# Kernel tuning notes

Measured on AMD Instinct MI355X. Metric: run time of the kernel, lower is better.

Reference implementation:

```python
import jax, jax.numpy as jnp
import numpy as np
from jax import lax

B, SEQ, PRED, CIN = 32, 336, 336, 7
ALL = SEQ + PRED
DM, DFF, NFFT, WIN, HOP = 64, 64, 64, 64, 8
NF = ALL // HOP + 1  # 85 STFT frames (center=True)
EL, CL, MARK = 2, 3, 4


def _conv2d(x, w, b, dil, pad):
    y = lax.conv_general_dilated(x, w, (1, 1), [(pad, pad), (pad, pad)],
                                 rhs_dilation=(dil, dil),
                                 dimension_numbers=('NCHW', 'OIHW', 'NCHW'))
    return y + b[None, :, None, None]


def _cconv(xr, xi, wr, wi, br, bi, dil, pad):
    # complex conv: (conv_r + i*conv_i)(xr + i*xi)
    rr = _conv2d(xr, wr, br, dil, pad)
    ii = _conv2d(xi, wi, bi, dil, pad)
    ri = _conv2d(xi, wr, br, dil, pad)
    ir = _conv2d(xr, wi, bi, dil, pad)
    return rr - ii, ri + ir


def _block(x, p):
    # x: [B, ALL, DM]; STFT per channel series (vectorized over B*DM, no python batch loop)
    xp = jnp.pad(x.transpose(0, 2, 1), ((0, 0), (0, 0), (NFFT // 2, NFFT // 2)), mode='reflect')
    idx = jnp.arange(NF)[:, None] * HOP + jnp.arange(NFFT)[None, :]
    win = 0.5 - 0.5 * jnp.cos(2.0 * jnp.pi * jnp.arange(WIN, dtype=jnp.float32) / WIN)  # periodic hann
    frames = xp[:, :, idx] * win  # [B, DM, NF, NFFT]
    S = jnp.fft.fft(frames, axis=-1) / jnp.sqrt(jnp.float32(NFFT))  # normalized=True (ortho)
    Sr = S.real.transpose(0, 1, 3, 2).astype(jnp.float32)  # [B, DM, NFFT, NF]
    Si = S.imag.transpose(0, 1, 3, 2).astype(jnp.float32)
    # complex 'qk' attention: compl_mul1d('ijxk,ijyk->ijxy', S, S)
    qk_r = jnp.einsum('bnxk,bnyk->bnxy', Sr, Sr) - jnp.einsum('bnxk,bnyk->bnxy', Si, Si)
    qk_i = jnp.einsum('bnxk,bnyk->bnxy', Sr, Si) + jnp.einsum('bnxk,bnyk->bnxy', Si, Sr)
    g_r = jax.nn.sigmoid(qk_r)
    g_i = jax.nn.sigmoid(qk_i)
    ar = jnp.einsum('bnxy,bnyz->bnxz', g_r, Sr) - jnp.einsum('bnxy,bnyz->bnxz', g_i, Si)
    ai = jnp.einsum('bnxy,bnyz->bnxz', g_r, Si) + jnp.einsum('bnxy,bnyz->bnxz', g_i, Sr)
    outs_r, outs_i = [], []
    yr, yi = _cconv(ar, ai, p['c0_wr'], p['c0_wi'], p['c0_br'], p['c0_bi'], 1, 0)
    outs_r.append(jax.nn.relu(yr)); outs_i.append(jax.nn.relu(yi))
    for k in range(1, CL):
        hr, hi = _cconv(ar, ai, p['cA_wr'][k - 1], p['cA_wi'][k - 1], p['cA_br'][k - 1], p['cA_bi'][k - 1], k, k)
        yr, yi = _cconv(hr, hi, p['cB_wr'][k - 1], p['cB_wi'][k - 1], p['cB_br'][k - 1], p['cB_bi'][k - 1], k, k)
        outs_r.append(jax.nn.relu(yr)); outs_i.append(jax.nn.relu(yi))
    mr = jnp.mean(jnp.stack(outs_r, -1), -1)
    mi = jnp.mean(jnp.stack(outs_i, -1), -1)
    y = mr * p['l0_w'][0, 0] + mi * p['l0_w'][0, 1] + p['l0_b'][0]  # Linear(2 -> 1) over (real, imag)
    y = y.mean(axis=2)  # mean over freq axis -> [B, DM, NF]
    y = jnp.einsum('bnf,af->bna', y, p['l2_w']) + p['l2_b']  # l2: NF -> ALL
    return y.transpose(0, 2, 1)  # [B, ALL, DM]


def _ln(x, g, b):
    m = x.mean(-1, keepdims=True)
    v = ((x - m) ** 2).mean(-1, keepdims=True)
    return (x - m) / jnp.sqrt(v + 1e-5) * g + b


def _forward(x_enc, x_mark_enc, tok_w, temp_w, pl_w, pl_b, ln_g, ln_b,
             c0_wr, c0_wi, c0_br, c0_bi, cA_wr, cA_wi, cA_br, cA_bi,
             cB_wr, cB_wi, cB_br, cB_bi, l0_w, l0_b, l2_w, l2_b,
             cv_w, cv_b, l1_w, l1_b, proj_w, proj_b):
    means = x_enc.mean(1, keepdims=True)
    xe = x_enc - means
    stdev = jnp.sqrt(xe.var(axis=1, keepdims=True) + 1e-5)
    xe = xe / stdev
    # DataEmbedding: circular token conv + sinusoidal PE + timeF linear (dropout=0)
    xv = jnp.pad(xe.transpose(0, 2, 1), ((0, 0), (0, 0), (1, 1)), mode='wrap')
    val = lax.conv_general_dilated(xv, tok_w, (1,), [(0, 0)],
                                   dimension_numbers=('NCH', 'OIH', 'NCH')).transpose(0, 2, 1)
    pos = jnp.arange(SEQ, dtype=jnp.float32)[:, None]
    div = jnp.exp(jnp.arange(0, DM, 2, dtype=jnp.float32) * (-np.log(10000.0) / DM))
    pe = jnp.zeros((SEQ, DM), jnp.float32).at[:, 0::2].set(jnp.sin(pos * div)).at[:, 1::2].set(jnp.cos(pos * div))
    enc = val + x_mark_enc @ temp_w.T + pe
    enc = jnp.einsum('btd,at->bad', enc, pl_w) + pl_b[None, :, None]  # predict_linear over time axis
    for l in range(EL):
        p = dict(c0_wr=c0_wr[l], c0_wi=c0_wi[l], c0_br=c0_br[l], c0_bi=c0_bi[l],
                 cA_wr=cA_wr[l], cA_wi=cA_wi[l], cA_br=cA_br[l], cA_bi=cA_bi[l],
                 cB_wr=cB_wr[l], cB_wi=cB_wi[l], cB_br=cB_br[l], cB_bi=cB_bi[l],
                 l0_w=l0_w[l], l0_b=l0_b[l], l2_w=l2_w[l], l2_b=l2_b[l])
        enc = _ln(_block(enc, p), ln_g, ln_b)
    # conv1d(in=ALL channels, kernel 3, stride 2, pad 1) over the d_model axis, then l1
    h = lax.conv_general_dilated(enc, cv_w, (2,), [(1, 1)],
                                 dimension_numbers=('NCH', 'OIH', 'NCH')) + cv_b[None, :, None]
    seq_series = (h @ l1_w.T)[..., 0] + l1_b[0]  # [B, ALL]
    dec = enc @ proj_w.T + proj_b
    dec = dec * stdev + means
    return dec[:, -PRED:, :], seq_series


def setup_inputs():
    key = jax.random.key(0)
    ks = jax.random.split(key, 24)
    def r(i, shape, s=0.02):
        return jax.random.normal(ks[i], shape, dtype=jnp.float32) * s
    return {
        'x_enc': jax.random.normal(ks[0], (B, SEQ, CIN), dtype=jnp.float32),
        'x_mark_enc': jax.random.normal(ks[1], (B, SEQ, MARK), dtype=jnp.float32),
        'x_dec': jax.random.normal(ks[2], (B, 48 + PRED, CIN), dtype=jnp.float32),
        'x_mark_dec': jax.random.normal(ks[3], (B, 48 + PRED, MARK), dtype=jnp.float32),
        'tok_w': r(4, (DM, CIN, 3), 0.1),
        'temp_w': r(5, (DM, MARK), 0.1),
        'pl_w': r(6, (ALL, SEQ), 0.05),
        'pl_b': jnp.zeros((ALL,), jnp.float32),
        'ln_g': jnp.ones((DM,), jnp.float32),
        'ln_b': jnp.zeros((DM,), jnp.float32),
        'c0_wr': r(7, (EL, DM, DM, 1, 1), 0.05),
        'c0_wi': r(8, (EL, DM, DM, 1, 1), 0.05),
        'c0_br': jnp.zeros((EL, DM), jnp.float32),
        'c0_bi': jnp.zeros((EL, DM), jnp.float32),
        'cA_wr': r(9, (EL, CL - 1, DFF, DM, 3, 3), 0.02),
        'cA_wi': r(10, (EL, CL - 1, DFF, DM, 3, 3), 0.02),
        'cA_br': jnp.zeros((EL, CL - 1, DFF), jnp.float32),
        'cA_bi': jnp.zeros((EL, CL - 1, DFF), jnp.float32),
        'cB_wr': r(11, (EL, CL - 1, DM, DFF, 3, 3), 0.02),
        'cB_wi': r(12, (EL, CL - 1, DM, DFF, 3, 3), 0.02),
        'cB_br': jnp.zeros((EL, CL - 1, DM), jnp.float32),
        'cB_bi': jnp.zeros((EL, CL - 1, DM), jnp.float32),
        'l0_w': r(13, (EL, 1, 2), 0.5),
        'l0_b': jnp.zeros((EL, 1), jnp.float32),
        'l2_w': r(14, (EL, ALL, NF), 0.05),
        'l2_b': jnp.zeros((EL, ALL), jnp.float32),
        'cv_w': r(15, (ALL, ALL, 3), 0.02),
        'cv_b': jnp.zeros((ALL,), jnp.float32),
        'l1_w': r(16, (1, DM // 2), 0.1),
        'l1_b': jnp.zeros((1,), jnp.float32),
        'proj_w': r(17, (CIN, DM), 0.1),
        'proj_b': jnp.zeros((CIN,), jnp.float32),
    }


def reference(x_enc, x_mark_enc, x_dec, x_mark_dec, tok_w, temp_w, pl_w, pl_b, ln_g, ln_b,
              c0_wr, c0_wi, c0_br, c0_bi, cA_wr, cA_wi, cA_br, cA_bi,
              cB_wr, cB_wi, cB_br, cB_bi, l0_w, l0_b, l2_w, l2_b,
              cv_w, cv_b, l1_w, l1_b, proj_w, proj_b):
    del x_dec, x_mark_dec  # unused in the forecast path
    return _forward(x_enc, x_mark_enc, tok_w, temp_w, pl_w, pl_b, ln_g, ln_b,
                    c0_wr, c0_wi, c0_br, c0_bi, cA_wr, cA_wi, cA_br, cA_bi,
                    cB_wr, cB_wi, cB_br, cB_bi, l0_w, l0_b, l2_w, l2_b,
                    cv_w, cv_b, l1_w, l1_b, proj_w, proj_b)
```

## Files before the change

### kernel.cpp

```cpp
#include <hip/hip_runtime.h>

typedef __attribute__((ext_vector_type(8))) short short8v;
typedef __attribute__((ext_vector_type(4))) float f32x4;
typedef __attribute__((ext_vector_type(16))) float f32x16;

static constexpr int Bt = 32;
static constexpr int SEQ = 336, PRED = 336, CIN = 7, ALLT = 672;
static constexpr int DM = 64, NFFT = 64, HOP = 8, NF = 85;
static constexpr int FPAD = 100;
static constexpr int MARK = 4;
static constexpr float INV3 = 1.0f / 3.0f;

__device__ inline short f2bf(float v) {
    unsigned u = __float_as_uint(v);
    u += 0x7fffu + ((u >> 16) & 1u);
    return (short)(u >> 16);
}
__device__ inline float bf2f(short h) {
    return __uint_as_float(((unsigned)(unsigned short)h) << 16);
}
__device__ inline int pack2(float r, float i) {
    return ((int)(unsigned short)f2bf(r)) | (((int)(unsigned short)f2bf(i)) << 16);
}
__device__ inline void async16(const int* g, short* l) {
    __builtin_amdgcn_global_load_lds(
        (const __attribute__((address_space(1))) unsigned int*)g,
        (__attribute__((address_space(3))) unsigned int*)l, 16, 0, 0);
}

__global__ __launch_bounds__(64) void k_stats(const float* __restrict__ x,
                                              float* __restrict__ mean,
                                              float* __restrict__ stdv) {
    int bc = blockIdx.x;
    int b = bc / CIN, c = bc % CIN;
    int lane = threadIdx.x;
    float s = 0.f, s2 = 0.f;
    for (int t = lane; t < SEQ; t += 64) {
        float v = x[(b * SEQ + t) * CIN + c];
        s += v; s2 += v * v;
    }
    for (int m = 32; m >= 1; m >>= 1) { s += __shfl_xor(s, m); s2 += __shfl_xor(s2, m); }
    if (lane == 0) {
        float mu = s / SEQ;
        float var = s2 / SEQ - mu * mu;
        mean[bc] = mu;
        stdv[bc] = sqrtf(var + 1e-5f);
    }
}

__global__ __launch_bounds__(256) void k_embed(const float* __restrict__ x,
                                               const float* __restrict__ mark,
                                               const float* __restrict__ tok_w,
                                               const float* __restrict__ temp_w,
                                               const float* __restrict__ mean,
                                               const float* __restrict__ stdv,
                                               float* __restrict__ enc0) {
    int i = blockIdx.x * 256 + threadIdx.x;
    if (i >= Bt * SEQ * DM) return;
    int d = i & 63;
    int t = (i >> 6) % SEQ;
    int b = i / (SEQ * DM);
    float val = 0.f;
    for (int c = 0; c < CIN; ++c) {
        float mu = mean[b * CIN + c];
        float is = 1.f / stdv[b * CIN + c];
        for (int j = 0; j < 3; ++j) {
            int tt = t + j - 1;
            if (tt < 0) tt += SEQ;
            if (tt >= SEQ) tt -= SEQ;
            float xv = (x[(b * SEQ + tt) * CIN + c] - mu) * is;
            val += xv * tok_w[(d * CIN + c) * 3 + j];
        }
    }
    float mk = 0.f;
    for (int m = 0; m < MARK; ++m) mk += mark[(b * SEQ + t) * MARK + m] * temp_w[d * MARK + m];
    float div = expf(-(float)(d & ~1) * (9.210340371976184f / (float)DM));
    float arg = (float)t * div;
    float pe = (d & 1) ? cosf(arg) : sinf(arg);
    enc0[i] = val + mk + pe;
}

__global__ __launch_bounds__(256) void k_plin2(const float* __restrict__ enc0,
                                               const float* __restrict__ pl_w,
                                               const float* __restrict__ pl_b,
                                               float* __restrict__ enc) {
    __shared__ float Et[56 * 64];
    __shared__ float Wt[56 * 49];
    int blk = blockIdx.x;
    int b = blk / 14, at = blk % 14;
    int abase = at * 48;
    int tid = threadIdx.x;
    int a0 = (tid & 15) * 3;
    int d0 = (tid >> 4) * 4;
    float acc[3][4];
#pragma unroll
    for (int q = 0; q < 3; ++q)
#pragma unroll
        for (int r = 0; r < 4; ++r) acc[q][r] = 0.f;
    for (int tc = 0; tc < 6; ++tc) {
        if (tc) __syncthreads();
        for (int i = tid; i < 56 * 64; i += 256)
            Et[i] = enc0[((size_t)b * SEQ + tc * 56) * DM + i];
        for (int i = tid; i < 48 * 56; i += 256) {
            int r = i / 56, c = i - r * 56;
            Wt[c * 49 + r] = pl_w[(size_t)(abase + r) * SEQ + tc * 56 + c];
        }
        __syncthreads();
#pragma unroll 4
        for (int t = 0; t < 56; ++t) {
            float4 e = *(const float4*)&Et[t * 64 + d0];
            float w0 = Wt[t * 49 + a0];
            float w1 = Wt[t * 49 + a0 + 1];
            float w2 = Wt[t * 49 + a0 + 2];
            acc[0][0] += w0 * e.x; acc[0][1] += w0 * e.y;
            acc[0][2] += w0 * e.z; acc[0][3] += w0 * e.w;
            acc[1][0] += w1 * e.x; acc[1][1] += w1 * e.y;
            acc[1][2] += w1 * e.z; acc[1][3] += w1 * e.w;
            acc[2][0] += w2 * e.x; acc[2][1] += w2 * e.y;
            acc[2][2] += w2 * e.z; acc[2][3] += w2 * e.w;
        }
    }
#pragma unroll
    for (int q = 0; q < 3; ++q) {
        int a = abase + a0 + q;
        float bias = pl_b[a];
        float4 o = {acc[q][0] + bias, acc[q][1] + bias, acc[q][2] + bias, acc[q][3] + bias};
        *(float4*)&enc[((size_t)b * ALLT + a) * DM + d0] = o;
    }
}

__global__ __launch_bounds__(256) void k_twprep(short* __restrict__ twg) {
    int idx = blockIdx.x * 256 + threadIdx.x;
    if (idx < 18432) {
        int arr = idx / 4608;
        int rem = idx - arr * 4608;
        int k = rem / 72, tt = rem - k * 72;
        float v = 0.f;
        if (tt < 64) {
            int m = (k * tt) & 63;
            float ang = (6.283185307179586f / 64.f) * (float)m;
            float c = (arr < 2) ? cosf(ang) : sinf(ang);
            v = (arr & 1) ? (c - bf2f(f2bf(c))) : c;
        }
        twg[idx] = f2bf(v);
    } else if (idx < 18432 + 64) {
        int tt = idx - 18432;
        float ang = (6.283185307179586f / 64.f) * (float)tt;
        ((float*)(twg + 18432))[tt] = (0.5f - 0.5f * cosf(ang)) * 0.125f;
    }
}

__global__ __launch_bounds__(256) void k_encT(const float* __restrict__ enc,
                                              float* __restrict__ encT) {
    __shared__ float tile[64][65];
    int b = blockIdx.x / 11, tt0 = (blockIdx.x % 11) * 64;
    int tid = threadIdx.x;
    int tx = tid & 63, ty = tid >> 6;
    for (int r = ty; r < 64; r += 4) {
        int t = tt0 + r;
        if (t < ALLT) tile[r][tx] = enc[((size_t)b * ALLT + t) * DM + tx];
    }
    __syncthreads();
    for (int r = ty; r < 64; r += 4) {
        int t = tt0 + tx;
        if (t < ALLT) encT[((size_t)b * DM + r) * ALLT + t] = tile[tx][r];
    }
}

__global__ __launch_bounds__(256) void k_padzero(int4* __restrict__ base, int nrows) {
    int idx = blockIdx.x * 256 + threadIdx.x;
    if (idx >= nrows * 15) return;
    int r = idx / 15, p = idx - r * 15;
    int f = (p < 2) ? p : (85 + p);
    base[(size_t)r * FPAD + f] = int4{0, 0, 0, 0};
}

__global__ __launch_bounds__(512) void k_stqka(const float* __restrict__ encT, int b0,
                                               int* __restrict__ Apk,
                                               const short* __restrict__ twg) {
    __shared__ __align__(16) short L[54272];
    constexpr int TCH = 0, TCL = 4608, TSH = 9216, TSL = 13824;
    constexpr int XWH = 18432, XWL = 25344;
    float* xp  = (float*)&L[32256];
    float* win = (float*)&L[33728];
    constexpr int SRH = 0, SIH = 6656, SRL = 13312, SIL = 19968;
    constexpr int STRH = 26624, STRL = 33536, STIH = 40448, STIL = 47360;
    constexpr int GRH = 0, GRL = 4608, GIH = 9216, GIL = 13824;

    int blk = blockIdx.x;
    int bn = (blk & 7) * (gridDim.x >> 3) + (blk >> 3);
    int bl = bn >> 6, n = bn & 63;
    int bg = b0 + bl;
    int tid = threadIdx.x;
    int lane = tid & 63, w = tid >> 6;
    int l31 = lane & 31, kg = lane >> 5;

    for (int i = tid; i < ALLT + NFFT; i += 512) {
        int j = i - 32;
        if (j < 0) j = -j;
        if (j > ALLT - 1) j = 2 * (ALLT - 1) - j;
        xp[i] = encT[(size_t)(bg * 64 + n) * ALLT + j];
    }
    for (int i = tid; i < 2304; i += 512)
        *(int4*)&L[i * 8] = ((const int4*)twg)[i];
    if (tid < 64) win[tid] = ((const float*)(twg + 18432))[tid];
    __syncthreads();
    for (int i = tid; i < 96 * 64; i += 512) {
        int f = i >> 6, tt = i & 63;
        float v = 0.f;
        if (f < 85) v = xp[f * HOP + tt] * win[tt];
        short vh = f2bf(v); short vl = f2bf(v - bf2f(vh));
        int o = f * 72 + tt;
        L[XWH + o] = vh; L[XWL + o] = vl;
    }
    __syncthreads();

    int kt = w & 1, ft = w >> 1;
    f32x16 sr, si;
#pragma unroll
    for (int r = 0; r < 16; ++r) { sr[r] = 0.f; si[r] = 0.f; }
    if (w < 6) {
#pragma unroll
        for (int tts = 0; tts < 4; ++tts) {
            int ko = (kt * 32 + l31) * 72 + tts * 16 + kg * 8;
            short8v ach = *(const short8v*)&L[TCH + ko];
            short8v acl = *(const short8v*)&L[TCL + ko];
            short8v ash = *(const short8v*)&L[TSH + ko];
            short8v asl = *(const short8v*)&L[TSL + ko];
            int bo = (ft * 32 + l31) * 72 + tts * 16 + kg * 8;
            short8v bh = *(const short8v*)&L[XWH + bo];
            short8v bl_ = *(const short8v*)&L[XWL + bo];
            sr = __builtin_amdgcn_mfma_f32_32x32x16_bf16(ach, bh, sr, 0, 0, 0);
            sr = __builtin_amdgcn_mfma_f32_32x32x16_bf16(acl, bh, sr, 0, 0, 0);
            sr = __builtin_amdgcn_mfma_f32_32x32x16_bf16(ach, bl_, sr, 0, 0, 0);
            si = __builtin_amdgcn_mfma_f32_32x32x16_bf16(ash, bh, si, 0, 0, 0);
            si = __builtin_amdgcn_mfma_f32_32x32x16_bf16(asl, bh, si, 0, 0, 0);
            si = __builtin_amdgcn_mfma_f32_32x32x16_bf16(ash, bl_, si, 0, 0, 0);
        }
    }
    __syncthreads();

    if (w < 6) {
        int fA = ft * 32 + l31;
#pragma unroll
        for (int rg = 0; rg < 4; ++rg) {
            int k0 = kt * 32 + 8 * rg + 4 * kg;
            short prh[4], prl[4], pih[4], pil[4];
#pragma unroll
            for (int q = 0; q < 4; ++q) {
                int r = rg * 4 + q;
                float sv = sr[r], iv = -si[r];
                short rh = f2bf(sv); short rl = f2bf(sv - bf2f(rh));
                short ih = f2bf(iv); short il = f2bf(iv - bf2f(ih));
                prh[q] = rh; prl[q] = rl; pih[q] = ih; pil[q] = il;
                L[SRH + (k0 + q) * 104 + fA] = rh; L[SRL + (k0 + q) * 104 + fA] = rl;
                L[SIH + (k0 + q) * 104 + fA] = ih; L[SIL + (k0 + q) * 104 + fA] = il;
            }
            *(long long*)&L[STRH + fA * 72 + k0] = *(long long*)prh;
            *(long long*)&L[STRL + fA * 72 + k0] = *(long long*)prl;
            *(long long*)&L[STIH + fA * 72 + k0] = *(long long*)pih;
            *(long long*)&L[STIL + fA * 72 + k0] = *(long long*)pil;
        }
    }
    __syncthreads();

    int mh = w >> 1, nh = w & 1;
    f32x16 P, Q, R;
#pragma unroll
    for (int r = 0; r < 16; ++r) { P[r] = 0.f; Q[r] = 0.f; R[r] = 0.f; }
    if (w < 4) {
#pragma unroll
        for (int f0 = 0; f0 < 96; f0 += 16) {
            int ka = f0 + kg * 8;
            int ra = (mh * 32 + l31) * 104 + ka;
            int rb = (nh * 32 + l31) * 104 + ka;
            short8v a_rh = *(const short8v*)&L[SRH + ra];
            short8v a_rl = *(const short8v*)&L[SRL + ra];
            short8v a_ih = *(const short8v*)&L[SIH + ra];
            short8v a_il = *(const short8v*)&L[SIL + ra];
            short8v b_rh = *(const short8v*)&L[SRH + rb];
            short8v b_rl = *(const short8v*)&L[SRL + rb];
            short8v b_ih = *(const short8v*)&L[SIH + rb];
            short8v b_il = *(const short8v*)&L[SIL + rb];
            P = __builtin_amdgcn_mfma_f32_32x32x16_bf16(a_rh, b_rh, P, 0, 0, 0);
            P = __builtin_amdgcn_mfma_f32_32x32x16_bf16(a_rl, b_rh, P, 0, 0, 0);
            P = __builtin_amdgcn_mfma_f32_32x32x16_bf16(a_rh, b_rl, P, 0, 0, 0);
            Q = __builtin_amdgcn_mfma_f32_32x32x16_bf16(a_ih, b_ih, Q, 0, 0, 0);
            Q = __builtin_amdgcn_mfma_f32_32x32x16_bf16(a_il, b_ih, Q, 0, 0, 0);
            Q = __builtin_amdgcn_mfma_f32_32x32x16_bf16(a_ih, b_il, Q, 0, 0, 0);
            R = __builtin_amdgcn_mfma_f32_32x32x16_bf16(a_rh, b_ih, R, 0, 0, 0);
            R = __builtin_amdgcn_mfma_f32_32x32x16_bf16(a_rl, b_ih, R, 0, 0, 0);
            R = __builtin_amdgcn_mfma_f32_32x32x16_bf16(a_rh, b_il, R, 0, 0, 0);
            R = __builtin_amdgcn_mfma_f32_32x32x16_bf16(a_ih, b_rh, R, 0, 0, 0);
            R = __builtin_amdgcn_mfma_f32_32x32x16_bf16(a_il, b_rh, R, 0, 0, 0);
            R = __builtin_amdgcn_mfma_f32_32x32x16_bf16(a_ih, b_rl, R, 0, 0, 0);
        }
    }
    __syncthreads();

    if (w < 4) {
        int y = nh * 32 + l31;
#pragma unroll
        for (int r = 0; r < 16; ++r) {
            int x = mh * 32 + (r & 3) + 8 * (r >> 2) + 4 * kg;
            float gr = 1.f / (1.f + __expf(-(P[r] - Q[r])));
            float gi = 1.f / (1.f + __expf(-R[r]));
            short gh = f2bf(gr); short gl = f2bf(gr - bf2f(gh));
            short jh = f2bf(gi); short jl = f2bf(gi - bf2f(jh));
            L[GRH + x * 72 + y] = gh; L[GRL + x * 72 + y] = gl;
            L[GIH + x * 72 + y] = jh; L[GIL + x * 72 + y] = jl;
        }
    }
    __syncthreads();

    int mt = w >> 1, nx = w & 1;
    f32x16 u1, u2, u3;
#pragma unroll
    for (int r = 0; r < 16; ++r) { u1[r] = 0.f; u2[r] = 0.f; u3[r] = 0.f; }
    if (w < 6) {
#pragma unroll
        for (int y0 = 0; y0 < 64; y0 += 16) {
            int kb = y0 + kg * 8;
            int gb = (nx * 32 + l31) * 72 + kb;
            short8v bgrh = *(const short8v*)&L[GRH + gb];
            short8v bgrl = *(const short8v*)&L[GRL + gb];
            short8v bgih = *(const short8v*)&L[GIH + gb];
            short8v bgil = *(const short8v*)&L[GIL + gb];
            int sa = (mt * 32 + l31) * 72 + kb;
            short8v arh = *(const short8v*)&L[STRH + sa];
            short8v arl = *(const short8v*)&L[STRL + sa];
            short8v aih = *(const short8v*)&L[STIH + sa];
            short8v ail = *(const short8v*)&L[STIL + sa];
            u1 = __builtin_amdgcn_mfma_f32_32x32x16_bf16(arh, bgrh, u1, 0, 0, 0);
            u1 = __builtin_amdgcn_mfma_f32_32x32x16_bf16(arl, bgrh, u1, 0, 0, 0);
            u1 = __builtin_amdgcn_mfma_f32_32x32x16_bf16(arh, bgrl, u1, 0, 0, 0);
            u2 = __builtin_amdgcn_mfma_f32_32x32x16_bf16(aih, bgih, u2, 0, 0, 0);
            u2 = __builtin_amdgcn_mfma_f32_32x32x16_bf16(ail, bgih, u2, 0, 0, 0);
            u2 = __builtin_amdgcn_mfma_f32_32x32x16_bf16(aih, bgil, u2, 0, 0, 0);
            u3 = __builtin_amdgcn_mfma_f32_32x32x16_bf16(aih, bgrh, u3, 0, 0, 0);
            u3 = __builtin_amdgcn_mfma_f32_32x32x16_bf16(ail, bgrh, u3, 0, 0, 0);
            u3 = __builtin_amdgcn_mfma_f32_32x32x16_bf16(aih, bgrl, u3, 0, 0, 0);
            u3 = __builtin_amdgcn_mfma_f32_32x32x16_bf16(arh, bgih, u3, 0, 0, 0);
            u3 = __builtin_amdgcn_mfma_f32_32x32x16_bf16(arl, bgih, u3, 0, 0, 0);
            u3 = __builtin_amdgcn_mfma_f32_32x32x16_bf16(arh, bgil, u3, 0, 0, 0);
        }
    }
    if (w < 6) {
        size_t pkbase = ((size_t)(bl * 16 + (n >> 2)) * 64) * FPAD * 4 + (n & 3);
        int x2 = nx * 32 + l31;
#pragma unroll
        for (int r = 0; r < 16; ++r) {
            int z = mt * 32 + (r & 3) + 8 * (r >> 2) + 4 * kg;
            if (z < 85)
                Apk[pkbase + ((size_t)x2 * FPAD + z + 2) * 4] = pack2(u1[r] - u2[r], u3[r]);
        }
    }
}

__global__ __launch_bounds__(256) void k_wprep(const float* __restrict__ cA_wr,
                                               const float* __restrict__ cA_wi,
                                               const float* __restrict__ cB_wr,
                                               const float* __restrict__ cB_wi,
                                               const float* __restrict__ c0_wr,
                                               const float* __restrict__ c0_wi,
                                               short* __restrict__ wt) {
    int idx = blockIdx.x * 256 + threadIdx.x;
    if (idx >= 1245184) return;
    int c32 = idx & 31;
    int m = (idx >> 5) & 127;
    int ci_l = c32 >> 1;
    int part = c32 & 1;
    int co = m & 63;
    const float *wr, *wi;
    size_t woff;
    bool lo = false;
    int chunk;
    if (idx < 1179648) {
        chunk = (idx >> 12) & 3;
        int tap = (idx >> 14) % 9;
        int conv = idx / 147456;
        int l = conv >> 2, k1 = (conv >> 1) & 1, ab = conv & 1;
        int ci = chunk * 16 + ci_l;
        woff = (((size_t)(l * 2 + k1) * 64 + co) * 64 + ci) * 9 + tap;
        wr = ab ? cB_wr : cA_wr;
        wi = ab ? cB_wi : cA_wi;
    } else {
        int i2 = idx - 1179648;
        chunk = (i2 >> 12) & 3;
        lo = (i2 >> 14) & 1;
        int l = i2 >> 15;
        int ci = chunk * 16 + ci_l;
        woff = ((size_t)(l * 64 + co)) * 64 + ci;
        wr = c0_wr; wi = c0_wi;
    }
    float a = wr[woff], bb = wi[woff];
    float v = (m < 64) ? (part ? -bb : a) : (part ? a : bb);
    if (lo) v = v - bf2f(f2bf(v));
    wt[idx] = f2bf(v);
}

__global__ __launch_bounds__(256, 4) void k_conv3p(const int* __restrict__ in_pk,
                                                   const short* __restrict__ wt,
                                                   const float* __restrict__ b_r,
                                                   const float* __restrict__ b_i,
                                                   int K, int mode,
                                                   const float* __restrict__ l0w,
                                                   int* __restrict__ out_pk,
                                                   float* __restrict__ yfull) {
    __shared__ __align__(16) short inT[2][1200 * 8];
    int blk = blockIdx.x;
    int swz = (blk & 7) * (gridDim.x >> 3) + (blk >> 3);
    int b = swz >> 6, x0 = swz & 63;
    int tid = threadIdx.x;
    int lane = tid & 63, wid = tid >> 6;
    int wrow = wid & 1, wcol = wid >> 1;
    int l15 = lane & 15, g = lane >> 4;

#define STAGE(CC, BUFI)                                                       \
    do {                                                                      \
        _Pragma("unroll")                                                     \
        for (int it = 0; it < 5; ++it) {                                      \
            int idx = tid + it * 256;                                         \
            if (idx < 1200) {                                                 \
                int f = idx % FPAD;                                           \
                int rc = idx / FPAD;                                          \
                int xr = rc >> 2, cg = rc & 3;                                \
                int xg = x0 + (xr - 1) * K;                                   \
                if ((unsigned)xg < 64u) {                                     \
                    const int* src = in_pk +                                  \
                        (((size_t)((b * 16 + (CC) * 4 + cg) * 64 + xg)) * FPAD + f) * 4; \
                    async16(src, &inT[BUFI][(wid * 64 + it * 256) * 8]);      \
                }                                                             \
            }                                                                 \
        }                                                                     \
    } while (0)

    { int* p = (int*)&inT[0][0];
      for (int i = tid; i < 2 * 1200 * 4; i += 256) p[i] = 0; }
    __syncthreads();

    f32x4 acc[4][3];
#pragma unroll
    for (int a = 0; a < 4; ++a)
#pragma unroll
        for (int j = 0; j < 3; ++j) acc[a][j] = f32x4{0.f, 0.f, 0.f, 0.f};

    STAGE(0, 0);
    __syncthreads();

    int cur = 0;
    for (int chunk = 0; chunk < 4; ++chunk) {
        if (chunk == 0) STAGE(1, 1);
        else if (chunk == 1) STAGE(2, 0);
        else if (chunk == 2) STAGE(3, 1);
        const short* bb = &inT[cur][0];
#pragma unroll
        for (int u = 0; u < 3; ++u) {
#pragma unroll
            for (int v = 0; v < 3; ++v) {
                int tap = u * 3 + v;
                short8v afr[4];
#pragma unroll
                for (int a = 0; a < 4; ++a) {
                    int tile = (a < 2) ? (wrow * 2 + a) : (wrow * 2 + a + 2);
                    const short* ap = wt + ((((size_t)tap * 4 + chunk) * 8 + tile) * 16 + l15) * 32 + g * 8;
                    afr[a] = *(const short8v*)ap;
                }
                short8v bfr[3];
#pragma unroll
                for (int j = 0; j < 3; ++j) {
                    int fs2 = (wcol * 3 + j) * 16 + l15 + (v - 1) * K + 2;
                    bfr[j] = *(const short8v*)&bb[((u * 4 + g) * FPAD + fs2) * 8];
                }
#pragma unroll
                for (int a = 0; a < 4; ++a)
#pragma unroll
                    for (int j = 0; j < 3; ++j)
                        acc[a][j] = __builtin_amdgcn_mfma_f32_16x16x32_bf16(afr[a], bfr[j],
                                                                            acc[a][j], 0, 0, 0);
            }
        }
        __syncthreads();
        cur ^= 1;
    }
#undef STAGE

    float w0 = 0.f, w1 = 0.f;
    if (mode == 1) { w0 = l0w[0]; w1 = l0w[1]; }
#pragma unroll
    for (int a = 0; a < 2; ++a) {
#pragma unroll
        for (int j = 0; j < 3; ++j) {
            int f = (wcol * 3 + j) * 16 + l15;
            if (f < NF) {
                if (mode == 0) {
                    int4 o;
#pragma unroll
                    for (int reg = 0; reg < 4; ++reg) {
                        int co = (wrow * 2 + a) * 16 + g * 4 + reg;
                        float vrq = acc[a][j][reg]     + b_r[co] - b_i[co];
                        float viq = acc[a + 2][j][reg] + b_r[co] + b_i[co];
                        ((int*)&o)[reg] = pack2(vrq, viq);
                    }
                    int co4 = (wrow * 2 + a) * 4 + g;
                    ((int4*)out_pk)[((size_t)((b * 16 + co4) * 64 + x0)) * FPAD + f + 2] = o;
                } else {
#pragma unroll
                    for (int reg = 0; reg < 4; ++reg) {
                        int co = (wrow * 2 + a) * 16 + g * 4 + reg;
                        float vrq = acc[a][j][reg]     + b_r[co] - b_i[co];
                        float viq = acc[a + 2][j][reg] + b_r[co] + b_i[co];
                        size_t o = ((size_t)(b * 64 + co) * 64 + x0) * NF + f;
                        yfull[o] += (fmaxf(vrq, 0.f) * w0 + fmaxf(viq, 0.f) * w1) * INV3;
                    }
                }
            }
        }
    }
}

__global__ __launch_bounds__(256, 4) void k_c0m(const int* __restrict__ Apk,
                                                const short* __restrict__ wt,
                                                const float* __restrict__ b_r,
                                                const float* __restrict__ b_i,
                                                const float* __restrict__ l0w,
                                                float* __restrict__ yfull) {
    __shared__ __align__(16) short inT[100 * 40];
    int blk = blockIdx.x;
    int swz = (blk & 7) * (gridDim.x >> 3) + (blk >> 3);
    int b = swz >> 6, x0 = swz & 63;
    int tid = threadIdx.x;
    int lane = tid & 63, wid = tid >> 6;
    int wrow = wid & 1, wcol = wid >> 1;
    int l15 = lane & 15, g = lane >> 4;

    f32x4 acc[4][3];
#pragma unroll
    for (int a = 0; a < 4; ++a)
#pragma unroll
        for (int j = 0; j < 3; ++j) acc[a][j] = f32x4{0.f, 0.f, 0.f, 0.f};

    for (int chunk = 0; chunk < 4; ++chunk) {
        if (chunk > 0) __syncthreads();
        for (int idx = tid; idx < 400; idx += 256) {
            int f = idx % FPAD;
            int cg = idx / FPAD;
            size_t s4 = ((size_t)((b * 16 + chunk * 4 + cg) * 64 + x0)) * FPAD + f;
            int4 dh = ((const int4*)Apk)[s4];
            *(int4*)&inT[f * 40 + cg * 8] = dh;
        }
        __syncthreads();
#pragma unroll
        for (int wtap = 0; wtap < 2; ++wtap) {
            short8v afr[4];
#pragma unroll
            for (int a = 0; a < 4; ++a) {
                int tile = (a < 2) ? (wrow * 2 + a) : (wrow * 2 + a + 2);
                const short* ap = wt + ((((size_t)wtap * 4 + chunk) * 8 + tile) * 16 + l15) * 32 + g * 8;
                afr[a] = *(const short8v*)ap;
            }
            short8v bfr[3];
#pragma unroll
            for (int j = 0; j < 3; ++j) {
                int fs = (wcol * 3 + j) * 16 + l15 + 2;
                bfr[j] = *(const short8v*)&inT[fs * 40 + g * 8];
            }
#pragma unroll
            for (int a = 0; a < 4; ++a)
#pragma unroll
                for (int j = 0; j < 3; ++j)
                    acc[a][j] = __builtin_amdgcn_mfma_f32_16x16x32_bf16(afr[a], bfr[j],
                                                                        acc[a][j], 0, 0, 0);
        }
    }

    float w0 = l0w[0], w1 = l0w[1];
#pragma unroll
    for (int a = 0; a < 2; ++a) {
#pragma unroll
        for (int j = 0; j < 3; ++j) {
            int f = (wcol * 3 + j) * 16 + l15;
            if (f < NF) {
#pragma unroll
                for (int reg = 0; reg < 4; ++reg) {
                    int co = (wrow * 2 + a) * 16 + g * 4 + reg;
                    float vrq = acc[a][j][reg]     + b_r[co] - b_i[co];
                    float viq = acc[a + 2][j][reg] + b_r[co] + b_i[co];
                    size_t o = ((size_t)(b * 64 + co) * 64 + x0) * NF + f;
                    yfull[o] = (fmaxf(vrq, 0.f) * w0 + fmaxf(viq, 0.f) * w1) * INV3;
                }
            }
        }
    }
}

__global__ __launch_bounds__(256) void k_reduce2(const float* __restrict__ yfull,
                                                 const float* __restrict__ l0b,
                                                 float* __restrict__ y2) {
    __shared__ float fs[3][85];
    int bn = blockIdx.x;
    int tid = threadIdx.x;
    const float* p = yfull + (size_t)bn * 64 * 85;
    if (tid < 255) {
        int f = tid % 85, g = tid / 85;
        float s = 0.f;
        for (int x = g; x < 64; x += 3) s += p[x * 85 + f];
        fs[g][f] = s;
    }
    __syncthreads();
    if (tid < 85)
        y2[(size_t)bn * 85 + tid] = (fs[0][tid] + fs[1][tid] + fs[2][tid]) * (1.f / 64.f) + l0b[0];
}

__global__ __launch_bounds__(64) void k_l2ln(const float* __restrict__ y2,
                                             const float* __restrict__ l2w,
                                             const float* __restrict__ l2b,
                                             const float* __restrict__ g,
                                             const float* __restrict__ be,
                                             float* __restrict__ enc, int b0) {
    int bl = blockIdx.x / ALLT;
    int a = blockIdx.x % ALLT;
    int d = threadIdx.x;
    const float* wp = l2w + (size_t)a * NF;
    const float* yp = y2 + (size_t)(bl * 64 + d) * NF;
    float acc = l2b[a];
    for (int f = 0; f < NF; ++f) acc += yp[f] * wp[f];
    float s = acc, s2 = acc * acc;
    for (int m = 32; m >= 1; m >>= 1) { s += __shfl_xor(s, m); s2 += __shfl_xor(s2, m); }
    float mu = s * (1.f / 64.f);
    float var = s2 * (1.f / 64.f) - mu * mu;
    float rs = rsqrtf(var + 1e-5f);
    enc[((size_t)(b0 + bl) * ALLT + a) * DM + d] = (acc - mu) * rs * g[d] + be[d];
}

__global__ __launch_bounds__(256) void k_T(const float* __restrict__ enc,
                                           const float* __restrict__ l1w,
                                           float* __restrict__ T) {
    int i = blockIdx.x * 256 + threadIdx.x;
    if (i >= Bt * ALLT * 3) return;
    int j = i % 3;
    int rest = i / 3;
    int ci = rest % ALLT;
    int b = rest / ALLT;
    const float* e = enc + ((size_t)b * ALLT + ci) * DM;
    float s = 0.f;
    for (int hx = 0; hx < 32; ++hx) {
        int p = 2 * hx + j - 1;
        if (p >= 0 && p < DM) s += e[p] * l1w[hx];
    }
    T[i] = s;
}

__global__ __launch_bounds__(256) void k_seq(const float* __restrict__ T,
                                             const float* __restrict__ cvw,
                                             const float* __restrict__ cvb,
                                             const float* __restrict__ l1w,
                                             const float* __restrict__ l1b,
                                             float* __restrict__ out) {
    int i = blockIdx.x * 256 + threadIdx.x;
    if (i >= Bt * ALLT) return;
    int co = i % ALLT;
    int b = i / ALLT;
    float sl1 = 0.f;
    for (int hx = 0; hx < 32; ++hx) sl1 += l1w[hx];
    const float* tp = T + (size_t)b * ALLT * 3;
    const float* wp = cvw + (size_t)co * ALLT * 3;
    float s = 0.f;
    for (int q = 0; q < ALLT * 3; ++q) s += tp[q] * wp[q];
    out[i] = s + cvb[co] * sl1 + l1b[0];
}

__global__ __launch_bounds__(256) void k_dec(const float* __restrict__ enc,
                                             const float* __restrict__ pw,
                                             const float* __restrict__ pb,
                                             const float* __restrict__ mean,
                                             const float* __restrict__ stdv,
                                             float* __restrict__ out) {
    int i = blockIdx.x * 256 + threadIdx.x;
    if (i >= Bt * PRED * CIN) return;
    int c = i % CIN;
    int rest = i / CIN;
    int tt = rest % PRED;
    int b = rest / PRED;
    const float* e = enc + ((size_t)b * ALLT + SEQ + tt) * DM;
    const float* w = pw + c * DM;
    float s = pb[c];
    for (int d = 0; d < DM; ++d) s += e[d] * w[d];
    out[i] = s * stdv[b * CIN + c] + mean[b * CIN + c];
}

extern "C" void kernel_launch(void* const* d_in, const int* in_sizes, int n_in,
                              void* d_out, int out_size, void* d_ws, size_t ws_size,
                              hipStream_t stream) {
    (void)in_sizes; (void)n_in; (void)out_size;
    const float* x_enc  = (const float*)d_in[0];
    const float* x_mark = (const float*)d_in[1];
    const float* tok_w  = (const float*)d_in[4];
    const float* temp_w = (const float*)d_in[5];
    const float* pl_w   = (const float*)d_in[6];
    const float* pl_b   = (const float*)d_in[7];
    const float* ln_g   = (const float*)d_in[8];
    const float* ln_b   = (const float*)d_in[9];
    const float* c0_wr  = (const float*)d_in[10];
    const float* c0_wi  = (const float*)d_in[11];
    const float* c0_br  = (const float*)d_in[12];
    const float* c0_bi  = (const float*)d_in[13];
    const float* cA_wr  = (const float*)d_in[14];
    const float* cA_wi  = (const float*)d_in[15];
    const float* cA_br  = (const float*)d_in[16];
    const float* cA_bi  = (const float*)d_in[17];
    const float* cB_wr  = (const float*)d_in[18];
    const float* cB_wi  = (const float*)d_in[19];
    const float* cB_br  = (const float*)d_in[20];
    const float* cB_bi  = (const float*)d_in[21];
    const float* l0_w   = (const float*)d_in[22];
    const float* l0_b   = (const float*)d_in[23];
    const float* l2_w   = (const float*)d_in[24];
    const float* l2_b   = (const float*)d_in[25];
    const float* cv_w   = (const float*)d_in[26];
    const float* cv_b   = (const float*)d_in[27];
    const float* l1_w   = (const float*)d_in[28];
    const float* l1_b   = (const float*)d_in[29];
    const float* proj_w = (const float*)d_in[30];
    const float* proj_b = (const float*)d_in[31];

    float* out0 = (float*)d_out;
    float* out1 = out0 + (size_t)Bt * PRED * CIN;

    float* ws = (float*)d_ws;
    size_t off = 0;
    float* enc  = ws + off; off += (size_t)Bt * ALLT * DM;
    float* encT = ws + off; off += (size_t)Bt * ALLT * DM;
    float* enc0 = ws + off; off += (size_t)Bt * SEQ * DM;
    float* mean = ws + off; off += 256;
    float* stdv = ws + off; off += 256;
    short* wtbuf = (short*)(ws + off); off += 622592;
    short* twg   = (short*)(ws + off); off += 9600;

    const size_t perb = (size_t)DM * NFFT * NF;
    const size_t perbp = (size_t)16 * 64 * FPAD * 4;
    int Bc = 32;
    while (Bc > 1) {
        size_t need = (off + (size_t)Bc * (DM * NF + perb + 2 * perbp)) * sizeof(float);
        if (need <= ws_size) break;
        Bc >>= 1;
    }
    float* y2 = ws + off; off += (size_t)Bc * DM * NF;
    float* yfull = ws + off; off += (size_t)Bc * perb;
    int*   Apk = (int*)(ws + off); off += (size_t)Bc * perbp;
    int*   Hpk = (int*)(ws + off); off += (size_t)Bc * perbp;
    float* Tb = enc0;

    k_stats<<<Bt * CIN, 64, 0, stream>>>(x_enc, mean, stdv);
    k_twprep<<<(18432 + 64 + 255) / 256, 256, 0, stream>>>(twg);
    k_wprep<<<(1245184 + 255) / 256, 256, 0, stream>>>(cA_wr, cA_wi, cB_wr, cB_wi,
                                                       c0_wr, c0_wi, wtbuf);
    {
        int nrows = 2 * Bc * 16 * 64;
        k_padzero<<<(nrows * 15 + 255) / 256, 256, 0, stream>>>((int4*)Apk, nrows);
    }
    k_embed<<<(Bt * SEQ * DM + 255) / 256, 256, 0, stream>>>(x_enc, x_mark, tok_w, temp_w,
                                                             mean, stdv, enc0);
    k_plin2<<<Bt * 14, 256, 0, stream>>>(enc0, pl_w, pl_b, enc);

    for (int l = 0; l < 2; ++l) {
        for (int b0 = 0; b0 < Bt; b0 += Bc) {
            k_encT<<<Bt * 11, 256, 0, stream>>>(enc, encT);
            k_stqka<<<Bc * 64, 512, 0, stream>>>(encT, b0, Apk, twg);
            k_c0m<<<Bc * 64, 256, 0, stream>>>(Apk, wtbuf + 1179648 + (size_t)l * 32768,
                                               c0_br + l * 64, c0_bi + l * 64,
                                               l0_w + l * 2, yfull);
            for (int k = 1; k <= 2; ++k) {
                int convA = l * 4 + (k - 1) * 2;
                size_t boff = ((size_t)l * 2 + (k - 1)) * 64;
                k_conv3p<<<Bc * 64, 256, 0, stream>>>(Apk, wtbuf + (size_t)convA * 147456,
                                                      cA_br + boff, cA_bi + boff, k, 0,
                                                      l0_w + l * 2, Hpk, yfull);
                k_conv3p<<<Bc * 64, 256, 0, stream>>>(Hpk, wtbuf + (size_t)(convA + 1) * 147456,
                                                      cB_br + boff, cB_bi + boff, k, 1,
                                                      l0_w + l * 2, Hpk, yfull);
            }
            k_reduce2<<<Bc * 64, 256, 0, stream>>>(yfull, l0_b + l, y2);
            k_l2ln<<<Bc * ALLT, 64, 0, stream>>>(y2, l2_w + (size_t)l * ALLT * NF,
                                                 l2_b + (size_t)l * ALLT, ln_g, ln_b, enc, b0);
        }
    }

    k_T<<<(Bt * ALLT * 3 + 255) / 256, 256, 0, stream>>>(enc, l1_w, Tb);
    k_seq<<<(Bt * ALLT + 255) / 256, 256, 0, stream>>>(Tb, cv_w, cv_b, l1_w, l1_b, out1);
    k_dec<<<(Bt * PRED * CIN + 255) / 256, 256, 0, stream>>>(enc, proj_w, proj_b, mean, stdv, out0);
}
```

Before: 1.379 ms.

## Fuse 1x1 complex conv into first dilated conv, compute transposed STFT via MFMA

Removes the separate k_c0m kernel. The 1x1 c0 convolution now runs inside the first k_conv3p launch (MODE 2), at the centre tap, reusing the already staged input fragments, and that mode drops occupancy to 3 blocks. In the STFT kernel a second set of MFMAs computes the transposed spectrum directly, so the scattered 2-byte LDS stores become packed 8-byte stores. The cost is doubled STFT MFMA work and higher register pressure in the fused conv.

```diff
diff --git a/kernel.cpp b/kernel.cpp
--- a/kernel.cpp
+++ b/kernel.cpp
@@ -216,9 +216,9 @@
     __syncthreads();
 
     int kt = w & 1, ft = w >> 1;
-    f32x16 sr, si;
-#pragma unroll
-    for (int r = 0; r < 16; ++r) { sr[r] = 0.f; si[r] = 0.f; }
+    f32x16 sr, si, sr2, si2;
+#pragma unroll
+    for (int r = 0; r < 16; ++r) { sr[r] = 0.f; si[r] = 0.f; sr2[r] = 0.f; si2[r] = 0.f; }
     if (w < 6) {
 #pragma unroll
         for (int tts = 0; tts < 4; ++tts) {
@@ -236,30 +236,53 @@
             si = __builtin_amdgcn_mfma_f32_32x32x16_bf16(ash, bh, si, 0, 0, 0);
             si = __builtin_amdgcn_mfma_f32_32x32x16_bf16(asl, bh, si, 0, 0, 0);
             si = __builtin_amdgcn_mfma_f32_32x32x16_bf16(ash, bl_, si, 0, 0, 0);
+            sr2 = __builtin_amdgcn_mfma_f32_32x32x16_bf16(bh, ach, sr2, 0, 0, 0);
+            sr2 = __builtin_amdgcn_mfma_f32_32x32x16_bf16(bh, acl, sr2, 0, 0, 0);
+            sr2 = __builtin_amdgcn_mfma_f32_32x32x16_bf16(bl_, ach, sr2, 0, 0, 0);
+            si2 = __builtin_amdgcn_mfma_f32_32x32x16_bf16(bh, ash, si2, 0, 0, 0);
+            si2 = __builtin_amdgcn_mfma_f32_32x32x16_bf16(bh, asl, si2, 0, 0, 0);
+            si2 = __builtin_amdgcn_mfma_f32_32x32x16_bf16(bl_, ash, si2, 0, 0, 0);
         }
     }
     __syncthreads();
 
     if (w < 6) {
         int fA = ft * 32 + l31;
+        int kA = kt * 32 + l31;
 #pragma unroll
         for (int rg = 0; rg < 4; ++rg) {
-            int k0 = kt * 32 + 8 * rg + 4 * kg;
-            short prh[4], prl[4], pih[4], pil[4];
-#pragma unroll
-            for (int q = 0; q < 4; ++q) {
-                int r = rg * 4 + q;
-                float sv = sr[r], iv = -si[r];
-                short rh = f2bf(sv); short rl = f2bf(sv - bf2f(rh));
-                short ih = f2bf(iv); short il = f2bf(iv - bf2f(ih));
-                prh[q] = rh; prl[q] = rl; pih[q] = ih; pil[q] = il;
-                L[SRH + (k0 + q) * 104 + fA] = rh; L[SRL + (k0 + q) * 104 + fA] = rl;
-                L[SIH + (k0 + q) * 104 + fA] = ih; L[SIL + (k0 + q) * 104 + fA] = il;
+            {
+                int k0 = kt * 32 + 8 * rg + 4 * kg;
+                short prh[4], prl[4], pih[4], pil[4];
+#pragma unroll
+                for (int q = 0; q < 4; ++q) {
+                    int r = rg * 4 + q;
+                    float sv = sr[r], iv = -si[r];
+                    short rh = f2bf(sv); short rl = f2bf(sv - bf2f(rh));
+                    short ih = f2bf(iv); short il = f2bf(iv - bf2f(ih));
+                    prh[q] = rh; prl[q] = rl; pih[q] = ih; pil[q] = il;
+                }
+                *(long long*)&L[STRH + fA * 72 + k0] = *(long long*)prh;
+                *(long long*)&L[STRL + fA * 72 + k0] = *(long long*)prl;
+                *(long long*)&L[STIH + fA * 72 + k0] = *(long long*)pih;
+                *(long long*)&L[STIL + fA * 72 + k0] = *(long long*)pil;
             }
-            *(long long*)&L[STRH + fA * 72 + k0] = *(long long*)prh;
-            *(long long*)&L[STRL + fA * 72 + k0] = *(long long*)prl;
-            *(long long*)&L[STIH + fA * 72 + k0] = *(long long*)pih;
-            *(long long*)&L[STIL + fA * 72 + k0] = *(long long*)pil;
+            {
+                int f0 = ft * 32 + 8 * rg + 4 * kg;
+                short qrh[4], qrl[4], qih[4], qil[4];
+#pragma unroll
+                for (int q = 0; q < 4; ++q) {
+                    int r = rg * 4 + q;
+                    float sv = sr2[r], iv = -si2[r];
+                    short rh = f2bf(sv); short rl = f2bf(sv - bf2f(rh));
+                    short ih = f2bf(iv); short il = f2bf(iv - bf2f(ih));
+                    qrh[q] = rh; qrl[q] = rl; qih[q] = ih; qil[q] = il;
+                }
+                *(long long*)&L[SRH + kA * 104 + f0] = *(long long*)qrh;
+                *(long long*)&L[SRL + kA * 104 + f0] = *(long long*)qrl;
+                *(long long*)&L[SIH + kA * 104 + f0] = *(long long*)qih;
+                *(long long*)&L[SIL + kA * 104 + f0] = *(long long*)qil;
+            }
         }
     }
     __syncthreads();
@@ -399,14 +422,19 @@
     wt[idx] = f2bf(v);
 }
 
-__global__ __launch_bounds__(256, 4) void k_conv3p(const int* __restrict__ in_pk,
-                                                   const short* __restrict__ wt,
-                                                   const float* __restrict__ b_r,
-                                                   const float* __restrict__ b_i,
-                                                   int K, int mode,
-                                                   const float* __restrict__ l0w,
-                                                   int* __restrict__ out_pk,
-                                                   float* __restrict__ yfull) {
+template <int MODE>
+__global__ __launch_bounds__(256, (MODE == 2) ? 3 : 4)
+void k_conv3p(const int* __restrict__ in_pk,
+              const short* __restrict__ wt,
+              const float* __restrict__ b_r,
+              const float* __restrict__ b_i,
+              int K,
+              const float* __restrict__ l0w,
+              int* __restrict__ out_pk,
+              float* __restrict__ yfull,
+              const short* __restrict__ wt_c0,
+              const float* __restrict__ c0_br,
+              const float* __restrict__ c0_bi) {
     __shared__ __align__(16) short inT[2][1200 * 8];
     int blk = blockIdx.x;
     int swz = (blk & 7) * (gridDim.x >> 3) + (blk >> 3);
@@ -444,6 +472,13 @@
     for (int a = 0; a < 4; ++a)
 #pragma unroll
         for (int j = 0; j < 3; ++j) acc[a][j] = f32x4{0.f, 0.f, 0.f, 0.f};
+    f32x4 acc0[4][3];
+    if constexpr (MODE == 2) {
+#pragma unroll
+        for (int a = 0; a < 4; ++a)
+#pragma unroll
+            for (int j = 0; j < 3; ++j) acc0[a][j] = f32x4{0.f, 0.f, 0.f, 0.f};
+    }
 
     STAGE(0, 0);
     __syncthreads();
@@ -478,6 +513,27 @@
                     for (int j = 0; j < 3; ++j)
                         acc[a][j] = __builtin_amdgcn_mfma_f32_16x16x32_bf16(afr[a], bfr[j],
                                                                             acc[a][j], 0, 0, 0);
+                if constexpr (MODE == 2) {
+                    if (u == 1 && v == 1) {
+#pragma unroll
+                        for (int wtap = 0; wtap < 2; ++wtap) {
+                            short8v cfr[4];
+#pragma unroll
+                            for (int a = 0; a < 4; ++a) {
+                                int tile = (a < 2) ? (wrow * 2 + a) : (wrow * 2 + a + 2);
+                                const short* cp = wt_c0 +
+                                    ((((size_t)wtap * 4 + chunk) * 8 + tile) * 16 + l15) * 32 + g * 8;
+                                cfr[a] = *(const short8v*)cp;
+                            }
+#pragma unroll
+                            for (int a = 0; a < 4; ++a)
+#pragma unroll
+                                for (int j = 0; j < 3; ++j)
+                                    acc0[a][j] = __builtin_amdgcn_mfma_f32_16x16x32_bf16(
+                                        cfr[a], bfr[j], acc0[a][j], 0, 0, 0);
+                        }
+                    }
+                }
             }
         }
         __syncthreads();
@@ -486,14 +542,14 @@
 #undef STAGE
 
     float w0 = 0.f, w1 = 0.f;
-    if (mode == 1) { w0 = l0w[0]; w1 = l0w[1]; }
+    if (MODE != 0) { w0 = l0w[0]; w1 = l0w[1]; }
 #pragma unroll
     for (int a = 0; a < 2; ++a) {
 #pragma unroll
         for (int j = 0; j < 3; ++j) {
             int f = (wcol * 3 + j) * 16 + l15;
             if (f < NF) {
-                if (mode == 0) {
+                if constexpr (MODE == 0 || MODE == 2) {
                     int4 o;
 #pragma unroll
                     for (int reg = 0; reg < 4; ++reg) {
@@ -504,90 +560,26 @@
                     }
                     int co4 = (wrow * 2 + a) * 4 + g;
                     ((int4*)out_pk)[((size_t)((b * 16 + co4) * 64 + x0)) * FPAD + f + 2] = o;
-                } else {
+                }
+                if constexpr (MODE == 2) {
+#pragma unroll
+                    for (int reg = 0; reg < 4; ++reg) {
+                        int co = (wrow * 2 + a) * 16 + g * 4 + reg;
+                        float vrq = acc0[a][j][reg]     + c0_br[co] - c0_bi[co];
+                        float viq = acc0[a + 2][j][reg] + c0_br[co] + c0_bi[co];
+                        size_t oy = ((size_t)(b * 64 + co) * 64 + x0) * NF + f;
+                        yfull[oy] = (fmaxf(vrq, 0.f) * w0 + fmaxf(viq, 0.f) * w1) * INV3;
+                    }
+                }
+                if constexpr (MODE == 1) {
 #pragma unroll
                     for (int reg = 0; reg < 4; ++reg) {
                         int co = (wrow * 2 + a) * 16 + g * 4 + reg;
                         float vrq = acc[a][j][reg]     + b_r[co] - b_i[co];
                         float viq = acc[a + 2][j][reg] + b_r[co] + b_i[co];
-                        size_t o = ((size_t)(b * 64 + co) * 64 + x0) * NF + f;
-                        yfull[o] += (fmaxf(vrq, 0.f) * w0 + fmaxf(viq, 0.f) * w1) * INV3;
+                        size_t oy = ((size_t)(b * 64 + co) * 64 + x0) * NF + f;
+                        yfull[oy] += (fmaxf(vrq, 0.f) * w0 + fmaxf(viq, 0.f) * w1) * INV3;
                     }
-                }
-            }
-        }
-    }
-}
-
-__global__ __launch_bounds__(256, 4) void k_c0m(const int* __restrict__ Apk,
-                                                const short* __restrict__ wt,
-                                                const float* __restrict__ b_r,
-                                                const float* __restrict__ b_i,
-                                                const float* __restrict__ l0w,
-                                                float* __restrict__ yfull) {
-    __shared__ __align__(16) short inT[100 * 40];
-    int blk = blockIdx.x;
-    int swz = (blk & 7) * (gridDim.x >> 3) + (blk >> 3);
-    int b = swz >> 6, x0 = swz & 63;
-    int tid = threadIdx.x;
-    int lane = tid & 63, wid = tid >> 6;
-    int wrow = wid & 1, wcol = wid >> 1;
-    int l15 = lane & 15, g = lane >> 4;
-
-    f32x4 acc[4][3];
-#pragma unroll
-    for (int a = 0; a < 4; ++a)
-#pragma unroll
-        for (int j = 0; j < 3; ++j) acc[a][j] = f32x4{0.f, 0.f, 0.f, 0.f};
-
-    for (int chunk = 0; chunk < 4; ++chunk) {
-        if (chunk > 0) __syncthreads();
-        for (int idx = tid; idx < 400; idx += 256) {
-            int f = idx % FPAD;
-            int cg = idx / FPAD;
-            size_t s4 = ((size_t)((b * 16 + chunk * 4 + cg) * 64 + x0)) * FPAD + f;
-            int4 dh = ((const int4*)Apk)[s4];
-            *(int4*)&inT[f * 40 + cg * 8] = dh;
-        }
-        __syncthreads();
-#pragma unroll
-        for (int wtap = 0; wtap < 2; ++wtap) {
-            short8v afr[4];
-#pragma unroll
-            for (int a = 0; a < 4; ++a) {
-                int tile = (a < 2) ? (wrow * 2 + a) : (wrow * 2 + a + 2);
-                const short* ap = wt + ((((size_t)wtap * 4 + chunk) * 8 + tile) * 16 + l15) * 32 + g * 8;
-                afr[a] = *(const short8v*)ap;
-            }
-            short8v bfr[3];
-#pragma unroll
-            for (int j = 0; j < 3; ++j) {
-                int fs = (wcol * 3 + j) * 16 + l15 + 2;
-                bfr[j] = *(const short8v*)&inT[fs * 40 + g * 8];
-            }
-#pragma unroll
-            for (int a = 0; a < 4; ++a)
-#pragma unroll
-                for (int j = 0; j < 3; ++j)
-                    acc[a][j] = __builtin_amdgcn_mfma_f32_16x16x32_bf16(afr[a], bfr[j],
-                                                                        acc[a][j], 0, 0, 0);
-        }
-    }
-
-    float w0 = l0w[0], w1 = l0w[1];
-#pragma unroll
-    for (int a = 0; a < 2; ++a) {
-#pragma unroll
-        for (int j = 0; j < 3; ++j) {
-            int f = (wcol * 3 + j) * 16 + l15;
-            if (f < NF) {
-#pragma unroll
-                for (int reg = 0; reg < 4; ++reg) {
-                    int co = (wrow * 2 + a) * 16 + g * 4 + reg;
-                    float vrq = acc[a][j][reg]     + b_r[co] - b_i[co];
-                    float viq = acc[a + 2][j][reg] + b_r[co] + b_i[co];
-                    size_t o = ((size_t)(b * 64 + co) * 64 + x0) * NF + f;
-                    yfull[o] = (fmaxf(vrq, 0.f) * w0 + fmaxf(viq, 0.f) * w1) * INV3;
                 }
             }
         }
@@ -767,18 +759,22 @@
         for (int b0 = 0; b0 < Bt; b0 += Bc) {
             k_encT<<<Bt * 11, 256, 0, stream>>>(enc, encT);
             k_stqka<<<Bc * 64, 512, 0, stream>>>(encT, b0, Apk, twg);
-            k_c0m<<<Bc * 64, 256, 0, stream>>>(Apk, wtbuf + 1179648 + (size_t)l * 32768,
-                                               c0_br + l * 64, c0_bi + l * 64,
-                                               l0_w + l * 2, yfull);
+            const short* wt_c0 = wtbuf + 1179648 + (size_t)l * 32768;
             for (int k = 1; k <= 2; ++k) {
                 int convA = l * 4 + (k - 1) * 2;
                 size_t boff = ((size_t)l * 2 + (k - 1)) * 64;
-                k_conv3p<<<Bc * 64, 256, 0, stream>>>(Apk, wtbuf + (size_t)convA * 147456,
-                                                      cA_br + boff, cA_bi + boff, k, 0,
-                                                      l0_w + l * 2, Hpk, yfull);
-                k_conv3p<<<Bc * 64, 256, 0, stream>>>(Hpk, wtbuf + (size_t)(convA + 1) * 147456,
-                                                      cB_br + boff, cB_bi + boff, k, 1,
-                                                      l0_w + l * 2, Hpk, yfull);
+                if (k == 1) {
+                    k_conv3p<2><<<Bc * 64, 256, 0, stream>>>(
+                        Apk, wtbuf + (size_t)convA * 147456, cA_br + boff, cA_bi + boff,
+                        k, l0_w + l * 2, Hpk, yfull, wt_c0, c0_br + l * 64, c0_bi + l * 64);
+                } else {
+                    k_conv3p<0><<<Bc * 64, 256, 0, stream>>>(
+                        Apk, wtbuf + (size_t)convA * 147456, cA_br + boff, cA_bi + boff,
+                        k, l0_w + l * 2, Hpk, yfull, wt_c0, c0_br + l * 64, c0_bi + l * 64);
+                }
+                k_conv3p<1><<<Bc * 64, 256, 0, stream>>>(
+                    Hpk, wtbuf + (size_t)(convA + 1) * 147456, cB_br + boff, cB_bi + boff,
+                    k, l0_w + l * 2, Hpk, yfull, wt_c0, c0_br + l * 64, c0_bi + l * 64);
             }
             k_reduce2<<<Bc * 64, 256, 0, stream>>>(yfull, l0_b + l, y2);
             k_l2ln<<<Bc * ALLT, 64, 0, stream>>>(y2, l2_w + (size_t)l * ALLT * NF,
```

Result: slower. 1.485 ms (+7.7%).
